# Kernel optimization log

Measured on AMD Instinct MI355X. Metric: run time of the kernel, lower is better.

The kernel has to match this reference:

```python
import jax, jax.numpy as jnp
import numpy as np

N_NODES = 100000
N_EDGES = 3200000
NFEAT = 128
NHID = 128
NCLASS = 8
BN_EPS = 1e-5


def setup_inputs() -> dict:
    key = jax.random.key(0)
    ks = jax.random.split(key, 8)
    x = jax.random.normal(ks[0], (N_NODES, NFEAT), dtype=jnp.float32)
    edge_index = jax.random.randint(ks[1], (2, N_EDGES), 0, N_NODES, dtype=jnp.int64)
    # GCNConv params: weight [nfeat, nhid] (glorot), bias [nhid]
    lim = float(np.sqrt(6.0 / (NFEAT + NHID)))
    W = jax.random.uniform(ks[2], (NFEAT, NHID), minval=-lim, maxval=lim, dtype=jnp.float32)
    b_gc = jnp.zeros((NHID,), dtype=jnp.float32)
    # BatchNorm1d params
    gamma = jnp.ones((NHID,), dtype=jnp.float32)
    beta = jnp.zeros((NHID,), dtype=jnp.float32)
    # fc head: (nhid/2) -> nclass, xavier_uniform, zero bias
    lim2 = float(np.sqrt(6.0 / (NHID // 2 + NCLASS)))
    fc_w = jax.random.uniform(ks[3], (NCLASS, NHID // 2), minval=-lim2, maxval=lim2, dtype=jnp.float32)
    fc_b = jnp.zeros((NCLASS,), dtype=jnp.float32)
    return {"x": x, "edge_index": edge_index, "W": W, "b_gc": b_gc,
            "gamma": gamma, "beta": beta, "fc_w": fc_w, "fc_b": fc_b}


def _gcn_conv(x, edge_index, W, b):
    """PyG GCNConv: add self-loops, symmetric norm, linear, gather-scatter, bias."""
    N = x.shape[0]
    loops = jnp.arange(N, dtype=edge_index.dtype)
    src = jnp.concatenate([edge_index[0], loops])  # source (row / x_j)
    dst = jnp.concatenate([edge_index[1], loops])  # target (col / aggregation index)
    # degree of target nodes (edge weight = 1)
    deg = jax.ops.segment_sum(jnp.ones_like(dst, dtype=x.dtype), dst, num_segments=N)
    dinv = jnp.where(deg > 0, jax.lax.rsqrt(deg), 0.0)
    norm = dinv[src] * dinv[dst]  # [E+N]
    h = x @ W  # [N, nhid]
    msg = h[src] * norm[:, None]  # gather + scale
    out = jax.ops.segment_sum(msg, dst, num_segments=N)  # scatter-add
    return out + b


def _batchnorm(h, gamma, beta):
    mean = jnp.mean(h, axis=0)
    var = jnp.mean(jnp.square(h - mean), axis=0)  # biased, training-mode
    return gamma * (h - mean) * jax.lax.rsqrt(var + BN_EPS) + beta


def reference(x, edge_index, W, b_gc, gamma, beta, fc_w, fc_b):
    h = _gcn_conv(x, edge_index, W, b_gc)
    embed = _batchnorm(h, gamma, beta)
    half = embed.shape[1] // 2
    out = embed[:, :half] @ fc_w.T + fc_b
    return (out, embed)
```

## Files before the change

### kernel.cpp

```cpp
#include <hip/hip_runtime.h>
#include <hip/hip_bf16.h>
#include <math.h>

#define N_NODES 100000
#define N_EDGES 3200000
#define NFEAT 128
#define NHID 128
#define NCLASS 8
#define BN_EPS 1e-5f
#define NBC 391
#define PART_BLOCKS 782

typedef __attribute__((ext_vector_type(8))) short short8;
typedef __attribute__((ext_vector_type(4))) float f32x4;

__device__ __forceinline__ short f2bf(float f) {
    __hip_bfloat16 b = __float2bfloat16(f);
    return *reinterpret_cast<short*>(&b);
}
__device__ __forceinline__ float bf_lo(unsigned u) { return __uint_as_float(u << 16); }
__device__ __forceinline__ float bf_hi(unsigned u) { return __uint_as_float(u & 0xffff0000u); }


__global__ __launch_bounds__(256) void k_chist(const int* __restrict__ dst,
                                               int* __restrict__ ghist) {
    __shared__ int lh[NBC];
    const int tid = threadIdx.x;
    for (int i = tid; i < NBC; i += 256) lh[i] = 0;
    __syncthreads();
    const int4* dst4 = (const int4*)dst;
    const int q0 = blockIdx.x * 1024 + tid;
#pragma unroll
    for (int i = 0; i < 4; ++i) {
        int q = q0 + i * 256;
        if (q < N_EDGES / 4) {
            int4 d = dst4[q];
            atomicAdd(&lh[d.x >> 8], 1);
            atomicAdd(&lh[d.y >> 8], 1);
            atomicAdd(&lh[d.z >> 8], 1);
            atomicAdd(&lh[d.w >> 8], 1);
        }
    }
    __syncthreads();
    for (int i = tid; i < NBC; i += 256) {
        int c = lh[i];
        if (c) atomicAdd(&ghist[i], c);
    }
}

__global__ __launch_bounds__(512) void k_cscan(const int* __restrict__ ghist,
                                               int* __restrict__ coff,
                                               int* __restrict__ ccur,
                                               int* __restrict__ off,
                                               float* __restrict__ stats) {
    __shared__ int tmp[512];
    const int t = threadIdx.x;
    if (t < 256) stats[t] = 0.f;
    int v = (t < NBC) ? ghist[t] : 0;
    tmp[t] = v;
    __syncthreads();
    for (int d = 1; d < 512; d <<= 1) {
        int u = (t >= d) ? tmp[t - d] : 0;
        __syncthreads();
        tmp[t] += u;
        __syncthreads();
    }
    int excl = tmp[t] - v;
    if (t < NBC) {
        coff[t] = excl;
        ccur[t] = excl;
    }
    if (t == NBC - 1) {
        coff[NBC] = tmp[t];
        off[N_NODES] = tmp[t];
    }
}

__global__ __launch_bounds__(256) void k_part(const int* __restrict__ src,
                                              const int* __restrict__ dst,
                                              int* __restrict__ ccur,
                                              unsigned* __restrict__ epack) {
    __shared__ int lh[NBC];
    __shared__ int lbase[NBC];
    const int tid = threadIdx.x;
    for (int i = tid; i < NBC; i += 256) lh[i] = 0;
    __syncthreads();
    const int4* src4 = (const int4*)src;
    const int4* dst4 = (const int4*)dst;
    const int q0 = blockIdx.x * 1024 + tid;
    int4 sv[4], dv[4];
    int rk[16];
    bool val[4];
#pragma unroll
    for (int i = 0; i < 4; ++i) {
        int q = q0 + i * 256;
        val[i] = q < N_EDGES / 4;
        if (val[i]) {
            sv[i] = src4[q];
            dv[i] = dst4[q];
            rk[i * 4 + 0] = atomicAdd(&lh[dv[i].x >> 8], 1);
            rk[i * 4 + 1] = atomicAdd(&lh[dv[i].y >> 8], 1);
            rk[i * 4 + 2] = atomicAdd(&lh[dv[i].z >> 8], 1);
            rk[i * 4 + 3] = atomicAdd(&lh[dv[i].w >> 8], 1);
        }
    }
    __syncthreads();
    for (int i = tid; i < NBC; i += 256) {
        int c = lh[i];
        lbase[i] = c ? atomicAdd(&ccur[i], c) : 0;
    }
    __syncthreads();
#pragma unroll
    for (int i = 0; i < 4; ++i) {
        if (val[i]) {
            epack[lbase[dv[i].x >> 8] + rk[i * 4 + 0]] = ((unsigned)sv[i].x << 8) | (unsigned)(dv[i].x & 255);
            epack[lbase[dv[i].y >> 8] + rk[i * 4 + 1]] = ((unsigned)sv[i].y << 8) | (unsigned)(dv[i].y & 255);
            epack[lbase[dv[i].z >> 8] + rk[i * 4 + 2]] = ((unsigned)sv[i].z << 8) | (unsigned)(dv[i].z & 255);
            epack[lbase[dv[i].w >> 8] + rk[i * 4 + 3]] = ((unsigned)sv[i].w << 8) | (unsigned)(dv[i].w & 255);
        }
    }
}

__global__ __launch_bounds__(256) void k_fine(const unsigned* __restrict__ epack,
                                              const int* __restrict__ coff,
                                              int* __restrict__ off,
                                              float* __restrict__ dinv,
                                              int* __restrict__ esrc) {
    __shared__ int lh[256], lcur[256], lsc[256];
    const int tid = threadIdx.x;
    const int b = blockIdx.x;
    const int node0 = b << 8;
    const int span = min(256, N_NODES - node0);
    lh[tid] = 0;
    __syncthreads();
    const int lo = coff[b], hiEnd = coff[b + 1];
    for (int i = lo + tid; i < hiEnd; i += 256)
        atomicAdd(&lh[epack[i] & 255u], 1);
    __syncthreads();
    int v = lh[tid];
    lsc[tid] = v;
    __syncthreads();
    for (int d = 1; d < 256; d <<= 1) {
        int u = (tid >= d) ? lsc[tid - d] : 0;
        __syncthreads();
        lsc[tid] += u;
        __syncthreads();
    }
    int excl = lsc[tid] - v;
    lcur[tid] = excl;
    if (tid < span) {
        off[node0 + tid] = lo + excl;
        dinv[node0 + tid] = rsqrtf((float)(v + 1));
    }
    __syncthreads();
    for (int i = lo + tid; i < hiEnd; i += 256) {
        unsigned p = epack[i];
        int pos = atomicAdd(&lcur[p & 255u], 1);
        esrc[lo + pos] = (int)(p >> 8);
    }
}


__global__ void k_wt(const float* __restrict__ W, unsigned short* __restrict__ Wt,
                     uint4* __restrict__ hbz) {
    int idx = blockIdx.x * blockDim.x + threadIdx.x;
    if (idx >= NFEAT * NHID) return;
    if (idx < 16) hbz[idx] = (uint4){0u, 0u, 0u, 0u};
    int k = idx >> 7, n = idx & 127;
    Wt[n * NFEAT + k] = (unsigned short)f2bf(W[idx]);
}


#define WSTRIDE 136
__global__ __launch_bounds__(256) void k_gemm(const float* __restrict__ x,
                                              const unsigned short* __restrict__ Wt,
                                              const float* __restrict__ dinv,
                                              unsigned short* __restrict__ hb) {
    __shared__ short wlds[NHID * WSTRIDE];
    const int tid = threadIdx.x;

    const unsigned* Wt32 = (const unsigned*)Wt;
    unsigned* wl32 = (unsigned*)wlds;
#pragma unroll
    for (int i = 0; i < 32; ++i) {
        int d = tid + i * 256;
        int n = d >> 6, kp = d & 63;
        wl32[n * (WSTRIDE / 2) + kp] = Wt32[d];
    }
    __syncthreads();

    const int wid = tid >> 6, lane = tid & 63;
    const int qw = lane >> 4, lr = lane & 15;
    const int arow = blockIdx.x * 64 + wid * 16 + lr;
    const bool avalid = arow < N_NODES;

    short8 a[4];
#pragma unroll
    for (int ks = 0; ks < 4; ++ks) {
        if (avalid) {
            const float* p = x + (size_t)arow * NFEAT + ks * 32 + qw * 8;
            float4 v0 = *(const float4*)p;
            float4 v1 = *(const float4*)(p + 4);
            short8 t;
            t[0] = f2bf(v0.x); t[1] = f2bf(v0.y); t[2] = f2bf(v0.z); t[3] = f2bf(v0.w);
            t[4] = f2bf(v1.x); t[5] = f2bf(v1.y); t[6] = f2bf(v1.z); t[7] = f2bf(v1.w);
            a[ks] = t;
        } else {
            short8 t;
#pragma unroll
            for (int j = 0; j < 8; ++j) t[j] = 0;
            a[ks] = t;
        }
    }

    f32x4 acc[8];
#pragma unroll
    for (int nt = 0; nt < 8; ++nt) acc[nt] = (f32x4){0.f, 0.f, 0.f, 0.f};

#pragma unroll
    for (int nt = 0; nt < 8; ++nt) {
#pragma unroll
        for (int ks = 0; ks < 4; ++ks) {
            short8 bfr = *(const short8*)&wlds[(nt * 16 + lr) * WSTRIDE + ks * 32 + qw * 8];
            acc[nt] = __builtin_amdgcn_mfma_f32_16x16x32_bf16(a[ks], bfr, acc[nt], 0, 0, 0);
        }
    }

    const int rbase = blockIdx.x * 64 + wid * 16 + qw * 4;
    float dv[4];
#pragma unroll
    for (int j = 0; j < 4; ++j) dv[j] = (rbase + j < N_NODES) ? dinv[rbase + j] : 0.f;
#pragma unroll
    for (int j = 0; j < 4; ++j) {
        int r = rbase + j;
        if (r >= N_NODES) continue;
#pragma unroll
        for (int nt = 0; nt < 8; ++nt)
            hb[(size_t)r * NHID + nt * 16 + lr] = (unsigned short)f2bf(dv[j] * acc[nt][j]);
    }
}


__global__ __launch_bounds__(256) void k_agg(const int* __restrict__ off,
                                             const int* __restrict__ esrc,
                                             const float* __restrict__ dinv,
                                             const uint2* __restrict__ hbq,
                                             float4* __restrict__ agg4) {
    const int node = (blockIdx.x << 2) | (threadIdx.x >> 6);
    const int lane = threadIdx.x & 63;
    const int hl = lane >> 5;
    const int cl = lane & 31;
    if (node >= N_NODES) return;

    const float dn = dinv[node];
    const int self = hl ? N_NODES : node;
    uint2 u0 = hbq[(size_t)self * 32 + cl];
    float axA = bf_lo(u0.x), ayA = bf_hi(u0.x), azA = bf_lo(u0.y), awA = bf_hi(u0.y);
    float axB = 0.f, ayB = 0.f, azB = 0.f, awB = 0.f;

    const int begin = off[node], end = off[node + 1];
    for (int base = begin; base < end; base += 64) {
        int m = end - base;
        if (m > 64) m = 64;
        int sv = (lane < m) ? esrc[base + lane] : N_NODES;
        const int kmax = (m + 3) >> 2;
        for (int k = 0; k < kmax; ++k) {
            int sA = __shfl(sv, 4 * k + hl);
            int sB = __shfl(sv, 4 * k + 2 + hl);
            uint2 uA = hbq[(size_t)sA * 32 + cl];
            uint2 uB = hbq[(size_t)sB * 32 + cl];
            axA += bf_lo(uA.x); ayA += bf_hi(uA.x);
            azA += bf_lo(uA.y); awA += bf_hi(uA.y);
            axB += bf_lo(uB.x); ayB += bf_hi(uB.x);
            azB += bf_lo(uB.y); awB += bf_hi(uB.y);
        }
    }
    float ax = axA + axB, ay = ayA + ayB, az = azA + azB, aw = awA + awB;
    ax += __shfl_xor(ax, 32);
    ay += __shfl_xor(ay, 32);
    az += __shfl_xor(az, 32);
    aw += __shfl_xor(aw, 32);
    if (hl == 0) {
        float4 o;
        o.x = ax * dn; o.y = ay * dn; o.z = az * dn; o.w = aw * dn;
        agg4[(size_t)node * 32 + cl] = o;
    }
}


__global__ __launch_bounds__(256) void k_stats(const float* __restrict__ agg,
                                               float* __restrict__ stats) {
    const int cb = threadIdx.x & 31;
    const int rg = threadIdx.x >> 5;
    const float4* a4 = (const float4*)agg;
    float4 s = {0.f, 0.f, 0.f, 0.f}, s2 = {0.f, 0.f, 0.f, 0.f};
    for (int r = blockIdx.x * 8 + rg; r < N_NODES; r += gridDim.x * 8) {
        float4 v = a4[(size_t)r * 32 + cb];
        s.x += v.x; s.y += v.y; s.z += v.z; s.w += v.w;
        s2.x += v.x * v.x; s2.y += v.y * v.y; s2.z += v.z * v.z; s2.w += v.w * v.w;
    }
    __shared__ float4 ls[256], ls2[256];
    ls[threadIdx.x] = s;
    ls2[threadIdx.x] = s2;
    __syncthreads();
    if (rg == 0) {
        float4 ts = ls[cb], t2 = ls2[cb];
#pragma unroll
        for (int g = 1; g < 8; ++g) {
            float4 v = ls[g * 32 + cb], w = ls2[g * 32 + cb];
            ts.x += v.x; ts.y += v.y; ts.z += v.z; ts.w += v.w;
            t2.x += w.x; t2.y += w.y; t2.z += w.z; t2.w += w.w;
        }
        atomicAdd(&stats[cb * 4 + 0], ts.x);
        atomicAdd(&stats[cb * 4 + 1], ts.y);
        atomicAdd(&stats[cb * 4 + 2], ts.z);
        atomicAdd(&stats[cb * 4 + 3], ts.w);
        atomicAdd(&stats[128 + cb * 4 + 0], t2.x);
        atomicAdd(&stats[128 + cb * 4 + 1], t2.y);
        atomicAdd(&stats[128 + cb * 4 + 2], t2.z);
        atomicAdd(&stats[128 + cb * 4 + 3], t2.w);
    }
}

__global__ void k_bn_params(const float* __restrict__ stats,
                            const float* __restrict__ gamma,
                            const float* __restrict__ beta,
                            float* __restrict__ ss) {
    int c = threadIdx.x;
    if (c >= NHID) return;
    float mean = stats[c] / (float)N_NODES;
    float var = stats[128 + c] / (float)N_NODES - mean * mean;
    var = fmaxf(var, 0.f);
    float inv = rsqrtf(var + BN_EPS);
    float sc = gamma[c] * inv;
    ss[c] = sc;
    ss[128 + c] = beta[c] - mean * sc;
}


__global__ __launch_bounds__(256) void k_bnfc(float* __restrict__ embed,
                                              const float* __restrict__ ss,
                                              const float* __restrict__ fc_w,
                                              const float* __restrict__ fc_b,
                                              float* __restrict__ out) {
    __shared__ float se[64][68];
    __shared__ float sw[8][68];
    __shared__ float sb[8];
    const int tid = threadIdx.x;
    const int row0 = blockIdx.x * 64;
    {
        int d = tid;
        sw[d >> 6][d & 63] = fc_w[d];
        d = tid + 256;
        sw[d >> 6][d & 63] = fc_w[d];
        if (tid < 8) sb[tid] = fc_b[tid];
    }
    float4* ef4 = (float4*)embed;
    const float4* ssc4 = (const float4*)ss;
    const float4* ssh4 = (const float4*)(ss + 128);
#pragma unroll
    for (int i = 0; i < 8; ++i) {
        int d = tid + i * 256;
        int r = d >> 5;
        int cb = d & 31;
        int gr = row0 + r;
        if (gr < N_NODES) {
            float4 v = ef4[(size_t)gr * 32 + cb];
            float4 sc = ssc4[cb], sh = ssh4[cb];
            v.x = fmaf(v.x, sc.x, sh.x);
            v.y = fmaf(v.y, sc.y, sh.y);
            v.z = fmaf(v.z, sc.z, sh.z);
            v.w = fmaf(v.w, sc.w, sh.w);
            ef4[(size_t)gr * 32 + cb] = v;
            if (cb < 16) {
                se[r][cb * 4 + 0] = v.x; se[r][cb * 4 + 1] = v.y;
                se[r][cb * 4 + 2] = v.z; se[r][cb * 4 + 3] = v.w;
            }
        } else if (cb < 16) {
            se[r][cb * 4 + 0] = 0.f; se[r][cb * 4 + 1] = 0.f;
            se[r][cb * 4 + 2] = 0.f; se[r][cb * 4 + 3] = 0.f;
        }
    }
    __syncthreads();
    const int r = tid >> 2;
    const int j0 = (tid & 3) * 2;
    const int gr = row0 + r;
#pragma unroll
    for (int jj = 0; jj < 2; ++jj) {
        int j = j0 + jj;
        float s = sb[j];
#pragma unroll
        for (int k = 0; k < 64; ++k) s = fmaf(se[r][k], sw[j][k], s);
        if (gr < N_NODES) out[(size_t)gr * NCLASS + j] = s;
    }
}


extern "C" void kernel_launch(void* const* d_in, const int* in_sizes, int n_in,
                              void* d_out, int out_size, void* d_ws, size_t ws_size,
                              hipStream_t stream) {
    const float* x     = (const float*)d_in[0];
    const int*   ei    = (const int*)d_in[1];
    const float* W     = (const float*)d_in[2];
    const float* gamma = (const float*)d_in[4];
    const float* beta  = (const float*)d_in[5];
    const float* fc_w  = (const float*)d_in[6];
    const float* fc_b  = (const float*)d_in[7];

    const int* src = ei;
    const int* dst = ei + N_EDGES;

    float* out   = (float*)d_out;
    float* embed = (float*)d_out + (size_t)N_NODES * NCLASS;

    char* ws = (char*)d_ws;
    size_t o = 0;
    unsigned* epack = (unsigned*)(ws + o);          o += (size_t)N_EDGES * 4;
    unsigned short* hb = (unsigned short*)(ws + o); o += (size_t)(N_NODES + 1) * NHID * 2;
    o = (o + 255) & ~(size_t)255;
    int* esrc   = (int*)(ws + o);                   o += (size_t)N_EDGES * 4;
    int* off    = (int*)(ws + o);                   o += (size_t)(N_NODES + 1) * 4;
    float* dinv = (float*)(ws + o);                 o += (size_t)N_NODES * 4;
    unsigned short* Wt = (unsigned short*)(ws + o); o += (size_t)NFEAT * NHID * 2;
    float* stats = (float*)(ws + o);                o += 256 * 4;
    float* ss    = (float*)(ws + o);                o += 256 * 4;
    int* ghist   = (int*)(ws + o);                  o += NBC * 4;
    int* coff    = (int*)(ws + o);                  o += (NBC + 1) * 4;
    int* ccur    = (int*)(ws + o);                  o += NBC * 4;

    hipMemsetAsync(ghist, 0, NBC * 4, stream);

    k_chist<<<PART_BLOCKS, 256, 0, stream>>>(dst, ghist);
    k_cscan<<<1, 512, 0, stream>>>(ghist, coff, ccur, off, stats);
    k_part<<<PART_BLOCKS, 256, 0, stream>>>(src, dst, ccur, epack);
    k_fine<<<NBC, 256, 0, stream>>>(epack, coff, off, dinv, esrc);

    k_wt<<<(NFEAT * NHID + 255) / 256, 256, 0, stream>>>(W, Wt, (uint4*)(hb + (size_t)N_NODES * NHID));
    k_gemm<<<(N_NODES + 63) / 64, 256, 0, stream>>>(x, Wt, dinv, hb);

    k_agg<<<(N_NODES + 3) / 4, 256, 0, stream>>>(off, esrc, dinv, (const uint2*)hb, (float4*)embed);

    k_stats<<<512, 256, 0, stream>>>(embed, stats);
    k_bn_params<<<1, 128, 0, stream>>>(stats, gamma, beta, ss);
    k_bnfc<<<(N_NODES + 63) / 64, 256, 0, stream>>>(embed, ss, fc_w, fc_b, out);
}
```

Before: 313.2 us.

## Fuse weight transpose and BN-param kernels; widen aggregation gather to four streams

Folds the weight-transpose kernel into the histogram kernel as extra blocks, and folds the BN parameter computation into the stats kernel using a last-block ticket counter. Together these remove two kernel launches. The aggregation loop now keeps four independent gather streams with their own accumulators instead of two, so more loads are in flight per wave. The cost is higher register pressure in the aggregation kernel and an atomic ticket plus threadfence at the end of the stats kernel.

```diff
diff --git a/kernel.cpp b/kernel.cpp
--- a/kernel.cpp
+++ b/kernel.cpp
@@ -10,6 +10,7 @@
 #define BN_EPS 1e-5f
 #define NBC 391
 #define PART_BLOCKS 782
+#define WT_BLOCKS 64
 
 typedef __attribute__((ext_vector_type(8))) short short8;
 typedef __attribute__((ext_vector_type(4))) float f32x4;
@@ -23,7 +24,17 @@
 
 
 __global__ __launch_bounds__(256) void k_chist(const int* __restrict__ dst,
-                                               int* __restrict__ ghist) {
+                                               int* __restrict__ ghist,
+                                               const float* __restrict__ W,
+                                               unsigned short* __restrict__ Wt,
+                                               uint4* __restrict__ hbz) {
+    if (blockIdx.x >= PART_BLOCKS) {
+        int idx = (blockIdx.x - PART_BLOCKS) * 256 + threadIdx.x;
+        if (idx < 16) hbz[idx] = (uint4){0u, 0u, 0u, 0u};
+        int k = idx >> 7, n = idx & 127;
+        Wt[n * NFEAT + k] = (unsigned short)f2bf(W[idx]);
+        return;
+    }
     __shared__ int lh[NBC];
     const int tid = threadIdx.x;
     for (int i = tid; i < NBC; i += 256) lh[i] = 0;
@@ -52,10 +63,12 @@
                                                int* __restrict__ coff,
                                                int* __restrict__ ccur,
                                                int* __restrict__ off,
-                                               float* __restrict__ stats) {
+                                               float* __restrict__ stats,
+                                               int* __restrict__ ticket) {
     __shared__ int tmp[512];
     const int t = threadIdx.x;
     if (t < 256) stats[t] = 0.f;
+    if (t == 0) *ticket = 0;
     int v = (t < NBC) ? ghist[t] : 0;
     tmp[t] = v;
     __syncthreads();
@@ -161,16 +174,6 @@
 }
 
 
-__global__ void k_wt(const float* __restrict__ W, unsigned short* __restrict__ Wt,
-                     uint4* __restrict__ hbz) {
-    int idx = blockIdx.x * blockDim.x + threadIdx.x;
-    if (idx >= NFEAT * NHID) return;
-    if (idx < 16) hbz[idx] = (uint4){0u, 0u, 0u, 0u};
-    int k = idx >> 7, n = idx & 127;
-    Wt[n * NFEAT + k] = (unsigned short)f2bf(W[idx]);
-}
-
-
 #define WSTRIDE 136
 __global__ __launch_bounds__(256) void k_gemm(const float* __restrict__ x,
                                               const unsigned short* __restrict__ Wt,
@@ -255,27 +258,36 @@
     const float dn = dinv[node];
     const int self = hl ? N_NODES : node;
     uint2 u0 = hbq[(size_t)self * 32 + cl];
-    float axA = bf_lo(u0.x), ayA = bf_hi(u0.x), azA = bf_lo(u0.y), awA = bf_hi(u0.y);
-    float axB = 0.f, ayB = 0.f, azB = 0.f, awB = 0.f;
+    float aAx = bf_lo(u0.x), aAy = bf_hi(u0.x), aAz = bf_lo(u0.y), aAw = bf_hi(u0.y);
+    float aBx = 0.f, aBy = 0.f, aBz = 0.f, aBw = 0.f;
+    float aCx = 0.f, aCy = 0.f, aCz = 0.f, aCw = 0.f;
+    float aDx = 0.f, aDy = 0.f, aDz = 0.f, aDw = 0.f;
 
     const int begin = off[node], end = off[node + 1];
     for (int base = begin; base < end; base += 64) {
         int m = end - base;
         if (m > 64) m = 64;
         int sv = (lane < m) ? esrc[base + lane] : N_NODES;
-        const int kmax = (m + 3) >> 2;
+        const int kmax = (m + 7) >> 3;
         for (int k = 0; k < kmax; ++k) {
-            int sA = __shfl(sv, 4 * k + hl);
-            int sB = __shfl(sv, 4 * k + 2 + hl);
+            int sA = __shfl(sv, 8 * k + 0 + hl);
+            int sB = __shfl(sv, 8 * k + 2 + hl);
+            int sC = __shfl(sv, 8 * k + 4 + hl);
+            int sD = __shfl(sv, 8 * k + 6 + hl);
             uint2 uA = hbq[(size_t)sA * 32 + cl];
             uint2 uB = hbq[(size_t)sB * 32 + cl];
-            axA += bf_lo(uA.x); ayA += bf_hi(uA.x);
-            azA += bf_lo(uA.y); awA += bf_hi(uA.y);
-            axB += bf_lo(uB.x); ayB += bf_hi(uB.x);
-            azB += bf_lo(uB.y); awB += bf_hi(uB.y);
-        }
-    }
-    float ax = axA + axB, ay = ayA + ayB, az = azA + azB, aw = awA + awB;
+            uint2 uC = hbq[(size_t)sC * 32 + cl];
+            uint2 uD = hbq[(size_t)sD * 32 + cl];
+            aAx += bf_lo(uA.x); aAy += bf_hi(uA.x); aAz += bf_lo(uA.y); aAw += bf_hi(uA.y);
+            aBx += bf_lo(uB.x); aBy += bf_hi(uB.x); aBz += bf_lo(uB.y); aBw += bf_hi(uB.y);
+            aCx += bf_lo(uC.x); aCy += bf_hi(uC.x); aCz += bf_lo(uC.y); aCw += bf_hi(uC.y);
+            aDx += bf_lo(uD.x); aDy += bf_hi(uD.x); aDz += bf_lo(uD.y); aDw += bf_hi(uD.y);
+        }
+    }
+    float ax = (aAx + aBx) + (aCx + aDx);
+    float ay = (aAy + aBy) + (aCy + aDy);
+    float az = (aAz + aBz) + (aCz + aDz);
+    float aw = (aAw + aBw) + (aCw + aDw);
     ax += __shfl_xor(ax, 32);
     ay += __shfl_xor(ay, 32);
     az += __shfl_xor(az, 32);
@@ -289,7 +301,11 @@
 
 
 __global__ __launch_bounds__(256) void k_stats(const float* __restrict__ agg,
-                                               float* __restrict__ stats) {
+                                               float* __restrict__ stats,
+                                               int* __restrict__ ticket,
+                                               const float* __restrict__ gamma,
+                                               const float* __restrict__ beta,
+                                               float* __restrict__ ss) {
     const int cb = threadIdx.x & 31;
     const int rg = threadIdx.x >> 5;
     const float4* a4 = (const float4*)agg;
@@ -300,6 +316,7 @@
         s2.x += v.x * v.x; s2.y += v.y * v.y; s2.z += v.z * v.z; s2.w += v.w * v.w;
     }
     __shared__ float4 ls[256], ls2[256];
+    __shared__ int lastflag;
     ls[threadIdx.x] = s;
     ls2[threadIdx.x] = s2;
     __syncthreads();
@@ -320,21 +337,22 @@
         atomicAdd(&stats[128 + cb * 4 + 2], t2.z);
         atomicAdd(&stats[128 + cb * 4 + 3], t2.w);
     }
-}
-
-__global__ void k_bn_params(const float* __restrict__ stats,
-                            const float* __restrict__ gamma,
-                            const float* __restrict__ beta,
-                            float* __restrict__ ss) {
-    int c = threadIdx.x;
-    if (c >= NHID) return;
-    float mean = stats[c] / (float)N_NODES;
-    float var = stats[128 + c] / (float)N_NODES - mean * mean;
-    var = fmaxf(var, 0.f);
-    float inv = rsqrtf(var + BN_EPS);
-    float sc = gamma[c] * inv;
-    ss[c] = sc;
-    ss[128 + c] = beta[c] - mean * sc;
+    __threadfence();
+    __syncthreads();
+    if (threadIdx.x == 0)
+        lastflag = (atomicAdd(ticket, 1) == (int)gridDim.x - 1) ? 1 : 0;
+    __syncthreads();
+    if (lastflag && threadIdx.x < NHID) {
+        int c = threadIdx.x;
+        float sum = atomicAdd(&stats[c], 0.f);
+        float sq  = atomicAdd(&stats[128 + c], 0.f);
+        float mean = sum / (float)N_NODES;
+        float var = fmaxf(sq / (float)N_NODES - mean * mean, 0.f);
+        float inv = rsqrtf(var + BN_EPS);
+        float sc = gamma[c] * inv;
+        ss[c] = sc;
+        ss[128 + c] = beta[c] - mean * sc;
+    }
 }
 
 
@@ -427,20 +445,21 @@
     int* ghist   = (int*)(ws + o);                  o += NBC * 4;
     int* coff    = (int*)(ws + o);                  o += (NBC + 1) * 4;
     int* ccur    = (int*)(ws + o);                  o += NBC * 4;
+    int* ticket  = (int*)(ws + o);                  o += 4;
 
     hipMemsetAsync(ghist, 0, NBC * 4, stream);
 
-    k_chist<<<PART_BLOCKS, 256, 0, stream>>>(dst, ghist);
-    k_cscan<<<1, 512, 0, stream>>>(ghist, coff, ccur, off, stats);
+    k_chist<<<PART_BLOCKS + WT_BLOCKS, 256, 0, stream>>>(dst, ghist, W, Wt,
+                                                         (uint4*)(hb + (size_t)N_NODES * NHID));
+    k_cscan<<<1, 512, 0, stream>>>(ghist, coff, ccur, off, stats, ticket);
     k_part<<<PART_BLOCKS, 256, 0, stream>>>(src, dst, ccur, epack);
     k_fine<<<NBC, 256, 0, stream>>>(epack, coff, off, dinv, esrc);
 
-    k_wt<<<(NFEAT * NHID + 255) / 256, 256, 0, stream>>>(W, Wt, (uint4*)(hb + (size_t)N_NODES * NHID));
     k_gemm<<<(N_NODES + 63) / 64, 256, 0, stream>>>(x, Wt, dinv, hb);
 
     k_agg<<<(N_NODES + 3) / 4, 256, 0, stream>>>(off, esrc, dinv, (const uint2*)hb, (float4*)embed);
 
-    k_stats<<<512, 256, 0, stream>>>(embed, stats);
-    k_bn_params<<<1, 128, 0, stream>>>(stats, gamma, beta, ss);
+    k_stats<<<512, 256, 0, stream>>>(embed, stats, ticket, gamma, beta, ss);
+
     k_bnfc<<<(N_NODES + 63) / 64, 256, 0, stream>>>(embed, ss, fc_w, fc_b, out);
 }
```

New measurement: 321.2 us. 1.03x slower.
